# Kernel tuning notes

Measured on AMD Instinct MI355X. Metric: run time of the kernel, lower is better.

Reference implementation:

```python
import jax, jax.numpy as jnp
import numpy as np

B, LP, LQ, H = 32, 2048, 512, 1024

def setup_inputs() -> dict:
    key = jax.random.key(0)
    k1, k2, k3, k4 = jax.random.split(key, 4)
    p_encode = jax.random.normal(k1, (B, LP, H), dtype=jnp.float32)
    q_encode = jax.random.normal(k2, (B, LQ, H), dtype=jnp.float32)
    # nn.Linear(H, H): weight [out, in], bias [out]
    bound = 1.0 / np.sqrt(H)
    G_weight = jax.random.uniform(k3, (H, H), dtype=jnp.float32, minval=-bound, maxval=bound)
    G_bias = jax.random.uniform(k4, (H,), dtype=jnp.float32, minval=-bound, maxval=bound)
    return {"p_encode": p_encode, "q_encode": q_encode, "G_weight": G_weight, "G_bias": G_bias}

def reference(p_encode, q_encode, G_weight, G_bias):
    # q_project = transpose(G(q_encode), -2, -1): [B, H, LQ]
    q_proj = jnp.einsum('bqh,oh->bqo', q_encode, G_weight) + G_bias  # [B, LQ, H]
    # att_matrix = bmm(p_encode, q_project^T): [B, LP, LQ]
    att = jnp.einsum('bph,bqh->bpq', p_encode, q_proj)
    # m_p = softmax over LQ (dim=-1) @ q_encode -> [B, LP, H]
    m_p = jnp.einsum('bpq,bqh->bph', jax.nn.softmax(att, axis=-1), q_encode)
    # m_q = softmax over LP (dim=-2), transposed, @ p_encode -> [B, LQ, H]
    m_q = jnp.einsum('bpq,bph->bqh', jax.nn.softmax(att, axis=-2), p_encode)
    return (m_p, m_q)
```

## Files before the change

### kernel.cpp

```cpp
#include <hip/hip_runtime.h>

typedef _Float16 half_t;
typedef _Float16 f16x8 __attribute__((ext_vector_type(8)));
typedef _Float16 f16x4 __attribute__((ext_vector_type(4)));
typedef float    f32x4 __attribute__((ext_vector_type(4)));
typedef float    f32x16 __attribute__((ext_vector_type(16)));

typedef const __attribute__((address_space(1))) void cg_void;
typedef __attribute__((address_space(3))) void lds_void;

#define BB 32
#define LP 2048
#define LQ 512
#define HH 1024

enum { M_QPROJ = 0, M_OUT32 = 1 };

__global__ void cvt16_k(const float* __restrict__ w, half_t* __restrict__ o) {
  long i = ((long)blockIdx.x * 256 + threadIdx.x) * 4;
  f32x4 v = *(const f32x4*)(w + i);
  f16x4 h;
  h[0] = (half_t)v[0]; h[1] = (half_t)v[1]; h[2] = (half_t)v[2]; h[3] = (half_t)v[3];
  *(f16x4*)(o + i) = h;
}

__global__ __launch_bounds__(256) void cvt2_k(const float* __restrict__ qe,
                                              half_t* __restrict__ q16o,
                                              half_t* __restrict__ qT16o,
                                              const float* __restrict__ pe,
                                              half_t* __restrict__ p16o,
                                              half_t* __restrict__ pT16o) {
  __shared__ half_t tile[64 * 64];
  const int byg = blockIdx.y;
  const float* in; half_t* rm; half_t* tr; int R, r0;
  if (byg < 8) { in = qe; rm = q16o; tr = qT16o; R = LQ; r0 = byg * 64; }
  else         { in = pe; rm = p16o; tr = pT16o; R = LP; r0 = (byg - 8) * 64; }
  const int C = HH;
  const long zb = blockIdx.z;
  const float* src = in + zb * (long)R * C;
  half_t* dstT = tr + zb * (long)C * R;
  half_t* dstR = rm + zb * (long)R * C;
  const int c0 = blockIdx.x * 64;
  const int t = threadIdx.x;
  const int cl = (t & 15) * 4;
  const int rl = t >> 4;
#pragma unroll
  for (int rr = 0; rr < 4; rr++) {
    int r = rr * 16 + rl;
    f32x4 v = *(const f32x4*)(src + (long)(r0 + r) * C + c0 + cl);
    f16x4 h;
#pragma unroll
    for (int j = 0; j < 4; j++) {
      h[j] = (half_t)v[j];
      int c = cl + j;
      tile[c * 64 + (r ^ (((c >> 3) & 7) << 3))] = h[j];
    }
    *(f16x4*)(dstR + (long)(r0 + r) * C + c0 + cl) = h;
  }
  __syncthreads();
  const int c = t >> 2;
  const int rch = (t & 3) * 16;
  const int m = (c >> 3) & 7;
  const int B0 = c * 64 + (rch ^ ((m << 3) & 48));
  const int hi = (m & 1) << 3;
  f16x8 g0 = *(const f16x8*)&tile[B0 + hi];
  f16x8 g1 = *(const f16x8*)&tile[B0 + (8 ^ hi)];
  half_t* dp = dstT + (long)(c0 + c) * R + r0 + rch;
  *(f16x8*)dp = g0;
  *(f16x8*)(dp + 8) = g1;
}

__global__ __launch_bounds__(256) void cfin_k(const float* __restrict__ pmg,
                                              const float* __restrict__ psg,
                                              float* __restrict__ cmax,
                                              float* __restrict__ cinv) {
  long i = (long)blockIdx.x * 256 + threadIdx.x;
  long b = i / LQ, q = i - b * LQ;
  const float* mp = pmg + (b * 16) * LQ + q;
  const float* sp = psg + (b * 16) * LQ + q;
  float m = -3e38f, s = 0.f;
#pragma unroll
  for (int t = 0; t < 16; t++) {
    float mm = mp[(long)t * LQ], ss = sp[(long)t * LQ];
    float nm = fmaxf(m, mm);
    s = s * __expf(m - nm) + ss * __expf(mm - nm);
    m = nm;
  }
  cmax[i] = m;
  cinv[i] = 1.f / s;
}

__global__ __launch_bounds__(256) void pq_k(const half_t* __restrict__ E,
                                            half_t* __restrict__ out,
                                            const float* __restrict__ pmg,
                                            const float* __restrict__ cmax,
                                            const float* __restrict__ cinv) {
  __shared__ half_t tile[64 * 64];
  const long zb = blockIdx.z;
  const half_t* src = E + zb * (long)LP * LQ;
  half_t* dst = out + zb * (long)LQ * LP;
  const int r0 = blockIdx.y * 64, c0 = blockIdx.x * 64;
  const int tIdx = r0 >> 7;
  const int t = threadIdx.x;
  const int cl = (t & 15) * 4;
  const int rl = t >> 4;
  f32x4 tm = *(const f32x4*)(pmg + ((long)zb * 16 + tIdx) * LQ + c0 + cl);
  f32x4 cm = *(const f32x4*)(cmax + (long)zb * LQ + c0 + cl);
  f32x4 ci = *(const f32x4*)(cinv + (long)zb * LQ + c0 + cl);
  float sc[4];
#pragma unroll
  for (int j = 0; j < 4; j++) sc[j] = __expf(tm[j] - cm[j]) * ci[j];
#pragma unroll
  for (int rr = 0; rr < 4; rr++) {
    int r = rr * 16 + rl;
    f16x4 v = *(const f16x4*)(src + (long)(r0 + r) * LQ + c0 + cl);
#pragma unroll
    for (int j = 0; j < 4; j++) {
      float x = (float)v[j] * sc[j];
      int c = cl + j;
      tile[c * 64 + (r ^ (((c >> 3) & 7) << 3))] = (half_t)x;
    }
  }
  __syncthreads();
  const int c = t >> 2;
  const int rch = (t & 3) * 16;
  const int m = (c >> 3) & 7;
  const int B0 = c * 64 + (rch ^ ((m << 3) & 48));
  const int hi = (m & 1) << 3;
  f16x8 g0 = *(const f16x8*)&tile[B0 + hi];
  f16x8 g1 = *(const f16x8*)&tile[B0 + (8 ^ hi)];
  half_t* dp = dst + (long)(c0 + c) * LP + r0 + rch;
  *(f16x8*)dp = g0;
  *(f16x8*)(dp + 8) = g1;
}

template<int ROWS>
__device__ __forceinline__ void stage_op(const half_t* src, int ld,
                                         half_t* lds_base, int wid, int lane) {
  const int goff = (((lane & 3) ^ ((lane >> 3) & 3)) << 3);
#pragma unroll
  for (int j = 0; j < ROWS / 128; ++j) {
    int row = j * 128 + wid * 16 + (lane >> 2);
    const half_t* g = src + (long)row * ld + goff;
    __builtin_amdgcn_global_load_lds((cg_void*)g,
        (lds_void*)(lds_base + j * 4096 + wid * 512), 16, 0, 0);
  }
}

__device__ __forceinline__ void xcd_swz(long lid, long nwg, long& out) {
  const long q8 = nwg >> 3, r8 = nwg & 7;
  const long xcd = lid & 7, rest = lid >> 3;
  out = (xcd < r8 ? xcd * (q8 + 1) : r8 * (q8 + 1) + (xcd - r8) * q8) + rest;
}

__global__ __launch_bounds__(512, 2) void attf_k(
    const half_t* __restrict__ Ap, const half_t* __restrict__ Bp,
    half_t* __restrict__ PpO, half_t* __restrict__ EO,
    float* __restrict__ pmg, float* __restrict__ psg) {
  __shared__ __align__(16) half_t As[3 * 4096];
  __shared__ __align__(16) half_t Bs[3 * 16384];
  __shared__ float rmL[4][128];
  __shared__ float cmL[2][512];
  __shared__ float rsL[4][128];
  __shared__ float csL[2][512];

  const int nby = gridDim.y;
  long lid;
  xcd_swz(blockIdx.y + (long)nby * blockIdx.z, (long)nby * gridDim.z, lid);
  const int by = (int)(lid % nby);
  const int bz = (int)(lid / nby);

  const int t0 = threadIdx.x;
  const int lane = t0 & 63;
  const int wid = t0 >> 6;
  const int wm = wid >> 2, wn = wid & 3;
  const int m0 = by * 128;

  const half_t* Abase = Ap + ((long)bz * LP + m0) * HH;
  const half_t* Bbase = Bp + (long)bz * LQ * HH;

  const int c5 = lane & 31, hi = lane >> 5;
  const int sx = (c5 >> 1) & 3;
  const int ofs0 = c5 * 32 + ((hi ^ sx) << 3);
  const int ofs1 = c5 * 32 + (((2 | hi) ^ sx) << 3);

  f32x16 acc[2][4] = {};
  const int NT = HH / 32;

#pragma unroll
  for (int tt = 0; tt < 2; ++tt) {
    stage_op<128>(Abase + tt * 32, HH, As + tt * 4096, wid, lane);
    stage_op<512>(Bbase + tt * 32, HH, Bs + tt * 16384, wid, lane);
  }

  for (int t = 0; t < NT; ++t) {
    if (t + 1 < NT) asm volatile("s_waitcnt vmcnt(5)" ::: "memory");
    else            asm volatile("s_waitcnt vmcnt(0)" ::: "memory");
    __builtin_amdgcn_s_barrier();
    asm volatile("" ::: "memory");

    const half_t* Au = As + (t % 3) * 4096;
    const half_t* Bu = Bs + (t % 3) * 16384;
    f16x8 af[2][2], bf[4][2];
#pragma unroll
    for (int mf = 0; mf < 2; ++mf) {
      const half_t* p = Au + (wm * 64 + mf * 32) * 32;
      af[mf][0] = *(const f16x8*)(p + ofs0);
      af[mf][1] = *(const f16x8*)(p + ofs1);
    }
#pragma unroll
    for (int nf = 0; nf < 4; ++nf) {
      const half_t* p = Bu + (wn * 128 + nf * 32) * 32;
      bf[nf][0] = *(const f16x8*)(p + ofs0);
      bf[nf][1] = *(const f16x8*)(p + ofs1);
    }
    if (t + 2 < NT) {
      const int u2 = (t + 2) % 3;
      stage_op<128>(Abase + (t + 2) * 32, HH, As + u2 * 4096, wid, lane);
      stage_op<512>(Bbase + (t + 2) * 32, HH, Bs + u2 * 16384, wid, lane);
    }
    __builtin_amdgcn_s_setprio(1);
#pragma unroll
    for (int mf = 0; mf < 2; ++mf)
#pragma unroll
      for (int nf = 0; nf < 4; ++nf) {
        acc[mf][nf] = __builtin_amdgcn_mfma_f32_32x32x16_f16(af[mf][0], bf[nf][0], acc[mf][nf], 0, 0, 0);
        acc[mf][nf] = __builtin_amdgcn_mfma_f32_32x32x16_f16(af[mf][1], bf[nf][1], acc[mf][nf], 0, 0, 0);
      }
    __builtin_amdgcn_s_setprio(0);
  }

  float rmv[2][16], cmv[4];
#pragma unroll
  for (int m = 0; m < 2; ++m)
#pragma unroll
    for (int r = 0; r < 16; ++r) {
      float v = fmaxf(fmaxf(acc[m][0][r], acc[m][1][r]), fmaxf(acc[m][2][r], acc[m][3][r]));
#pragma unroll
      for (int o = 1; o < 32; o <<= 1) v = fmaxf(v, __shfl_xor(v, o, 64));
      rmv[m][r] = v;
    }
#pragma unroll
  for (int n = 0; n < 4; ++n) {
    float v = acc[0][n][0];
#pragma unroll
    for (int m = 0; m < 2; ++m)
#pragma unroll
      for (int r = 0; r < 16; ++r) v = fmaxf(v, acc[m][n][r]);
    v = fmaxf(v, __shfl_xor(v, 32, 64));
    cmv[n] = v;
  }
  if (c5 < 16) {
#pragma unroll
    for (int m = 0; m < 2; ++m)
      rmL[wn][wm * 64 + m * 32 + (c5 & 3) + 8 * (c5 >> 2) + 4 * hi] = rmv[m][c5];
  }
  if (hi == 0) {
#pragma unroll
    for (int n = 0; n < 4; ++n) cmL[wm][wn * 128 + n * 32 + c5] = cmv[n];
  }
  __syncthreads();
  if (t0 < 128)
    rmL[0][t0] = fmaxf(fmaxf(rmL[0][t0], rmL[1][t0]), fmaxf(rmL[2][t0], rmL[3][t0]));
  {
    float cm2 = fmaxf(cmL[0][t0 & 511], cmL[1][t0 & 511]);
    cmL[0][t0 & 511] = cm2;
    pmg[((long)bz * 16 + by) * LQ + (t0 & 511)] = cm2;
  }
  __syncthreads();
#pragma unroll
  for (int m = 0; m < 2; ++m)
#pragma unroll
    for (int r = 0; r < 16; ++r)
      rmv[m][r] = rmL[0][wm * 64 + m * 32 + (r & 3) + 8 * (r >> 2) + 4 * hi];
#pragma unroll
  for (int n = 0; n < 4; ++n) cmv[n] = cmL[0][wn * 128 + n * 32 + c5];

  half_t* EB = EO + (long)bz * LP * LQ;
  float csW[4] = {0.f, 0.f, 0.f, 0.f};
  float rowS[2][16];
#pragma unroll
  for (int m = 0; m < 2; ++m)
#pragma unroll
    for (int r = 0; r < 16; ++r) {
      long grow = (long)(m0 + wm * 64 + m * 32 + (r & 3) + 8 * (r >> 2) + 4 * hi) * LQ;
      float s = 0.f;
#pragma unroll
      for (int n = 0; n < 4; ++n) {
        float a = acc[m][n][r];
        float e = __expf(a - cmv[n]);
        float p = __expf(a - rmv[m][r]);
        csW[n] += e;
        EB[grow + wn * 128 + n * 32 + c5] = (half_t)e;
        acc[m][n][r] = p;
        s += p;
      }
#pragma unroll
      for (int o = 1; o < 32; o <<= 1) s += __shfl_xor(s, o, 64);
      rowS[m][r] = s;
    }
#pragma unroll
  for (int n = 0; n < 4; ++n) csW[n] += __shfl_xor(csW[n], 32, 64);
  if (c5 < 16) {
#pragma unroll
    for (int m = 0; m < 2; ++m)
      rsL[wn][wm * 64 + m * 32 + (c5 & 3) + 8 * (c5 >> 2) + 4 * hi] = rowS[m][c5];
  }
  if (hi == 0) {
#pragma unroll
    for (int n = 0; n < 4; ++n) csL[wm][wn * 128 + n * 32 + c5] = csW[n];
  }
  __syncthreads();
  if (t0 < 128)
    rsL[0][t0] = 1.f / (rsL[0][t0] + rsL[1][t0] + rsL[2][t0] + rsL[3][t0]);
  psg[((long)bz * 16 + by) * LQ + (t0 & 511)] = csL[0][t0 & 511] + csL[1][t0 & 511];
  __syncthreads();

  half_t* PpB = PpO + (long)bz * LP * LQ;
#pragma unroll
  for (int m = 0; m < 2; ++m)
#pragma unroll
    for (int r = 0; r < 16; ++r) {
      int row = wm * 64 + m * 32 + (r & 3) + 8 * (r >> 2) + 4 * hi;
      long grow = (long)(m0 + row) * LQ;
      float ri = rsL[0][row];
#pragma unroll
      for (int n = 0; n < 4; ++n)
        PpB[grow + wn * 128 + n * 32 + c5] = (half_t)(acc[m][n][r] * ri);
    }
}

template<int MODE>
__device__ __forceinline__ void core8(const half_t* __restrict__ Ab,
                                      const half_t* __restrict__ Bb,
                                      void* __restrict__ cB,
                                      const float* __restrict__ biasB,
                                      int lda, int ldb, int ldc, int K) {
  __shared__ __align__(16) half_t As[3][8192];
  __shared__ __align__(16) half_t Bs[3][8192];

  const int t0 = threadIdx.x;
  const int lane = t0 & 63;
  const int wid = t0 >> 6;
  const int wm = wid >> 2, wn = wid & 3;
  const int fr = lane & 15, fs = lane >> 4;
  const int fbase = fr * 32 + ((fs ^ ((fr >> 1) & 3)) << 3);

  f32x4 acc[8][4] = {};
  const int NT = K >> 5;

  stage_op<256>(Ab, lda, As[0], wid, lane);
  stage_op<256>(Bb, ldb, Bs[0], wid, lane);
  stage_op<256>(Ab + 32, lda, As[1], wid, lane);
  stage_op<256>(Bb + 32, ldb, Bs[1], wid, lane);
  asm volatile("s_waitcnt vmcnt(4)" ::: "memory");
  __builtin_amdgcn_s_barrier();
  asm volatile("" ::: "memory");

  for (int t = 0; t < NT; ++t) {
    const half_t* Au = As[t % 3];
    const half_t* Bu = Bs[t % 3];
    f16x8 af[4], bf[4], ag[4];
#pragma unroll
    for (int mf = 0; mf < 4; ++mf)
      af[mf] = *(const f16x8*)&Au[(wm * 128 + mf * 16) * 32 + fbase];
#pragma unroll
    for (int nf = 0; nf < 4; ++nf)
      bf[nf] = *(const f16x8*)&Bu[(wn * 64 + nf * 16) * 32 + fbase];
    if (t + 2 < NT) stage_op<256>(Ab + (t + 2) * 32, lda, As[(t + 2) % 3], wid, lane);
    __builtin_amdgcn_s_barrier();
    asm volatile("" ::: "memory");
    __builtin_amdgcn_s_setprio(1);
#pragma unroll
    for (int mf = 0; mf < 4; ++mf)
#pragma unroll
      for (int nf = 0; nf < 4; ++nf)
        acc[mf][nf] = __builtin_amdgcn_mfma_f32_16x16x32_f16(af[mf], bf[nf], acc[mf][nf], 0, 0, 0);
    __builtin_amdgcn_s_setprio(0);
    __builtin_amdgcn_s_barrier();
    asm volatile("" ::: "memory");
#pragma unroll
    for (int mf = 0; mf < 4; ++mf)
      ag[mf] = *(const f16x8*)&Au[(wm * 128 + 64 + mf * 16) * 32 + fbase];
    if (t + 2 < NT) stage_op<256>(Bb + (t + 2) * 32, ldb, Bs[(t + 2) % 3], wid, lane);
    __builtin_amdgcn_s_setprio(1);
#pragma unroll
    for (int mf = 0; mf < 4; ++mf)
#pragma unroll
      for (int nf = 0; nf < 4; ++nf)
        acc[4 + mf][nf] = __builtin_amdgcn_mfma_f32_16x16x32_f16(ag[mf], bf[nf], acc[4 + mf][nf], 0, 0, 0);
    __builtin_amdgcn_s_setprio(0);
    if (t + 2 < NT)      asm volatile("s_waitcnt vmcnt(4)" ::: "memory");
    else if (t + 1 < NT) asm volatile("s_waitcnt vmcnt(0)" ::: "memory");
    __builtin_amdgcn_s_barrier();
    asm volatile("" ::: "memory");
  }

  const int r0 = (lane >> 4) * 4;
#pragma unroll
  for (int nf = 0; nf < 4; ++nf) {
    int col = wn * 64 + nf * 16 + fr;
    float bv = 0.f;
    if constexpr (MODE == M_QPROJ) bv = biasB[col];
#pragma unroll
    for (int i = 0; i < 8; ++i) {
      int row = wm * 128 + (i >> 2) * 64 + (i & 3) * 16 + r0;
#pragma unroll
      for (int j = 0; j < 4; j++) {
        if constexpr (MODE == M_QPROJ)
          ((half_t*)cB)[(long)(row + j) * ldc + col] = (half_t)(acc[i][nf][j] + bv);
        else
          ((float*)cB)[(long)(row + j) * ldc + col] = acc[i][nf][j];
      }
    }
  }
}

__global__ __launch_bounds__(512, 2) void gemmq_k(const half_t* __restrict__ q16,
                                                  const half_t* __restrict__ w16,
                                                  half_t* __restrict__ qpj,
                                                  const float* __restrict__ Gb) {
  long lid;
  xcd_swz(blockIdx.x + 4L * blockIdx.y, 4L * gridDim.y, lid);
  const int bx = (int)(lid % 4);
  const int by = (int)(lid / 4);
  core8<M_QPROJ>(q16 + (long)(by * 256) * HH,
                 w16 + (long)(bx * 256) * HH,
                 qpj + (long)(by * 256) * HH + bx * 256,
                 Gb + bx * 256, HH, HH, HH, HH);
}

__global__ __launch_bounds__(512, 2) void gemm2_k(
    const half_t* __restrict__ Pp, const half_t* __restrict__ qT16, float* __restrict__ m_p,
    const half_t* __restrict__ Pq, const half_t* __restrict__ pT16, float* __restrict__ m_q) {
  long lid;
  xcd_swz(blockIdx.x + 4L * (blockIdx.y + 10L * blockIdx.z), 4L * 10 * 32, lid);
  const int bx = (int)(lid % 4);
  const long tmp = lid / 4;
  const int by = (int)(tmp % 10);
  const int bz = (int)(tmp / 10);

  if (by < 2) {
    core8<M_OUT32>(Pq + (long)bz * LQ * LP + (long)(by * 256) * LP,
                   pT16 + (long)bz * HH * LP + (long)(bx * 256) * LP,
                   m_q + (long)bz * LQ * HH + (long)(by * 256) * HH + bx * 256,
                   nullptr, LP, LP, HH, LP);
  } else {
    const int py = by - 2;
    core8<M_OUT32>(Pp + (long)bz * LP * LQ + (long)(py * 256) * LQ,
                   qT16 + (long)bz * HH * LQ + (long)(bx * 256) * LQ,
                   m_p + (long)bz * LP * HH + (long)(py * 256) * HH + bx * 256,
                   nullptr, LQ, LQ, HH, LQ);
  }
}

extern "C" void kernel_launch(void* const* d_in, const int* in_sizes, int n_in,
                              void* d_out, int out_size, void* d_ws, size_t ws_size,
                              hipStream_t stream) {
  const float* p_enc = (const float*)d_in[0];
  const float* q_enc = (const float*)d_in[1];
  const float* Gw    = (const float*)d_in[2];
  const float* Gb    = (const float*)d_in[3];
  float* m_p = (float*)d_out;
  float* m_q = m_p + (long)BB * LP * HH;

  half_t* w16   = (half_t*)d_ws;
  half_t* q16   = w16 + (long)HH * HH;
  half_t* qT16  = q16 + (long)BB * LQ * HH;
  half_t* qpj16 = qT16 + (long)BB * HH * LQ;
  half_t* p16   = qpj16 + (long)BB * LQ * HH;
  half_t* pT16  = p16 + (long)BB * LP * HH;
  half_t* Pp    = pT16 + (long)BB * HH * LP;
  half_t* Ebuf  = Pp + (long)BB * LP * LQ;
  half_t* Pq    = Ebuf + (long)BB * LP * LQ;
  float*  cmaxb = (float*)(Pq + (long)BB * LQ * LP);
  float*  cinvb = cmaxb + (long)BB * LQ;
  float*  pmg   = cinvb + (long)BB * LQ;
  float*  psg   = pmg + (long)BB * 16 * LQ;

  cvt16_k<<<HH * HH / 1024, 256, 0, stream>>>(Gw, w16);

  cvt2_k<<<dim3(HH / 64, 40, BB), 256, 0, stream>>>(q_enc, q16, qT16, p_enc, p16, pT16);

  gemmq_k<<<dim3(4, 64, 1), 512, 0, stream>>>(q16, w16, qpj16, Gb);

  attf_k<<<dim3(1, LP / 128, BB), 512, 0, stream>>>(p16, qpj16, Pp, Ebuf, pmg, psg);

  cfin_k<<<BB * LQ / 256, 256, 0, stream>>>(pmg, psg, cmaxb, cinvb);
  pq_k<<<dim3(LQ / 64, LP / 64, BB), 256, 0, stream>>>(Ebuf, Pq, pmg, cmaxb, cinvb);

  gemm2_k<<<dim3(4, 10, BB), 512, 0, stream>>>(Pp, qT16, m_p, Pq, pT16, m_q);
}
```

Baseline: 564.9 us.

## Rework GEMM mainloop into 8-slot quarter-tile pipeline with K=64 stages

Replaces the 3-stage K=32 double-operand pipeline with an 8-slot LDS ring of half-tiles staged at K=64. Loads are issued in quarter-steps interleaved with four MFMA phases per iteration. LDS grows to 128KB per block, so launch bounds drop to one block per CU. The aim is deeper prefetch and finer-grained overlap of global-to-LDS loads with MFMA, at the cost of occupancy and more barriers per iteration.

```diff
diff --git a/kernel.cpp b/kernel.cpp
--- a/kernel.cpp
+++ b/kernel.cpp
@@ -330,109 +330,145 @@
     }
 }
 
+__device__ __forceinline__ void stage_half(const half_t* src, int ld, int k0,
+                                           half_t* slot, int half_id, int wid, int lane) {
+#pragma unroll
+  for (int j = 0; j < 2; ++j) {
+    int c = j * 512 + wid * 64 + lane;
+    int lr = c >> 3, sl = c & 7;
+    int gr = (lr & 63) + half_id * 64 + (lr >> 6) * 128;
+    const half_t* g = src + (long)gr * ld + k0 + (((sl ^ (lr & 7))) << 3);
+    __builtin_amdgcn_global_load_lds((cg_void*)g,
+        (lds_void*)(slot + j * 4096 + wid * 512), 16, 0, 0);
+  }
+}
+
+__device__ __forceinline__ void stage_s(int s, const half_t* Ab, const half_t* Bb,
+                                        int lda, int ldb, half_t* lds, int NT,
+                                        int wid, int lane) {
+  int ts = s >> 2;
+  if (ts >= NT) return;
+  int kind = s & 3;
+  half_t* slot = lds + (s & 7) * 8192;
+  int k0 = ts * 64;
+  if (kind == 0)      stage_half(Ab, lda, k0, slot, 0, wid, lane);
+  else if (kind == 1) stage_half(Bb, ldb, k0, slot, 0, wid, lane);
+  else if (kind == 2) stage_half(Bb, ldb, k0, slot, 1, wid, lane);
+  else                stage_half(Ab, lda, k0, slot, 1, wid, lane);
+}
+
 template<int MODE>
-__device__ __forceinline__ void core8(const half_t* __restrict__ Ab,
-                                      const half_t* __restrict__ Bb,
-                                      void* __restrict__ cB,
-                                      const float* __restrict__ biasB,
-                                      int lda, int ldb, int ldc, int K) {
-  __shared__ __align__(16) half_t As[3][8192];
-  __shared__ __align__(16) half_t Bs[3][8192];
-
+__device__ __forceinline__ void core8p(const half_t* __restrict__ Ab,
+                                       const half_t* __restrict__ Bb,
+                                       void* __restrict__ cB,
+                                       const float* __restrict__ biasB,
+                                       int lda, int ldb, int ldc, int K,
+                                       half_t* lds) {
   const int t0 = threadIdx.x;
   const int lane = t0 & 63;
   const int wid = t0 >> 6;
   const int wm = wid >> 2, wn = wid & 3;
   const int fr = lane & 15, fs = lane >> 4;
-  const int fbase = fr * 32 + ((fs ^ ((fr >> 1) & 3)) << 3);
 
   f32x4 acc[8][4] = {};
-  const int NT = K >> 5;
-
-  stage_op<256>(Ab, lda, As[0], wid, lane);
-  stage_op<256>(Bb, ldb, Bs[0], wid, lane);
-  stage_op<256>(Ab + 32, lda, As[1], wid, lane);
-  stage_op<256>(Bb + 32, ldb, Bs[1], wid, lane);
+  const int NT = K >> 6;
+
+#pragma unroll
+  for (int s = 0; s < 5; ++s) stage_s(s, Ab, Bb, lda, ldb, lds, NT, wid, lane);
   asm volatile("s_waitcnt vmcnt(4)" ::: "memory");
   __builtin_amdgcn_s_barrier();
   asm volatile("" ::: "memory");
 
   for (int t = 0; t < NT; ++t) {
-    const half_t* Au = As[t % 3];
-    const half_t* Bu = Bs[t % 3];
-    f16x8 af[4], bf[4], ag[4];
-#pragma unroll
-    for (int mf = 0; mf < 4; ++mf)
-      af[mf] = *(const f16x8*)&Au[(wm * 128 + mf * 16) * 32 + fbase];
-#pragma unroll
-    for (int nf = 0; nf < 4; ++nf)
-      bf[nf] = *(const f16x8*)&Bu[(wn * 64 + nf * 16) * 32 + fbase];
-    if (t + 2 < NT) stage_op<256>(Ab + (t + 2) * 32, lda, As[(t + 2) % 3], wid, lane);
-    __builtin_amdgcn_s_barrier();
-    asm volatile("" ::: "memory");
-    __builtin_amdgcn_s_setprio(1);
-#pragma unroll
-    for (int mf = 0; mf < 4; ++mf)
-#pragma unroll
-      for (int nf = 0; nf < 4; ++nf)
-        acc[mf][nf] = __builtin_amdgcn_mfma_f32_16x16x32_f16(af[mf], bf[nf], acc[mf][nf], 0, 0, 0);
-    __builtin_amdgcn_s_setprio(0);
-    __builtin_amdgcn_s_barrier();
-    asm volatile("" ::: "memory");
-#pragma unroll
-    for (int mf = 0; mf < 4; ++mf)
-      ag[mf] = *(const f16x8*)&Au[(wm * 128 + 64 + mf * 16) * 32 + fbase];
-    if (t + 2 < NT) stage_op<256>(Bb + (t + 2) * 32, ldb, Bs[(t + 2) % 3], wid, lane);
-    __builtin_amdgcn_s_setprio(1);
-#pragma unroll
-    for (int mf = 0; mf < 4; ++mf)
-#pragma unroll
-      for (int nf = 0; nf < 4; ++nf)
-        acc[4 + mf][nf] = __builtin_amdgcn_mfma_f32_16x16x32_f16(ag[mf], bf[nf], acc[4 + mf][nf], 0, 0, 0);
-    __builtin_amdgcn_s_setprio(0);
-    if (t + 2 < NT)      asm volatile("s_waitcnt vmcnt(4)" ::: "memory");
-    else if (t + 1 < NT) asm volatile("s_waitcnt vmcnt(0)" ::: "memory");
-    __builtin_amdgcn_s_barrier();
-    asm volatile("" ::: "memory");
-  }
-
-  const int r0 = (lane >> 4) * 4;
+    const int base4 = 4 * t;
+    const half_t* slotA0 = lds + ((base4) & 7) * 8192;
+    const half_t* slotB0 = lds + ((base4 + 1) & 7) * 8192;
+    const half_t* slotB1 = lds + ((base4 + 2) & 7) * 8192;
+    const half_t* slotA1 = lds + ((base4 + 3) & 7) * 8192;
+    const bool drain = (t + 2 >= NT);
+    f16x8 bf[4][2];
+#pragma unroll
+    for (int p = 0; p < 4; ++p) {
+      f16x8 af[2][2];
+      const half_t* aslot = (p < 2) ? slotA0 : slotA1;
+      const int lrbase = wm * 64 + (p & 1) * 32;
+#pragma unroll
+      for (int i = 0; i < 2; ++i) {
+        int lr = lrbase + i * 16 + fr;
+#pragma unroll
+        for (int kh = 0; kh < 2; ++kh)
+          af[i][kh] = *(const f16x8*)&aslot[lr * 64 + (((fs + 4 * kh) ^ (lr & 7)) << 3)];
+      }
+      if (p == 0) {
+        const half_t* bslot = (wn & 1) ? slotB1 : slotB0;
+#pragma unroll
+        for (int nf = 0; nf < 4; ++nf) {
+          int lr = (wn >> 1) * 64 + nf * 16 + fr;
+#pragma unroll
+          for (int kh = 0; kh < 2; ++kh)
+            bf[nf][kh] = *(const f16x8*)&bslot[lr * 64 + (((fs + 4 * kh) ^ (lr & 7)) << 3)];
+        }
+      }
+      stage_s(base4 + p + 5, Ab, Bb, lda, ldb, lds, NT, wid, lane);
+      if (drain) asm volatile("s_waitcnt vmcnt(0)" ::: "memory");
+      else       asm volatile("s_waitcnt vmcnt(4)" ::: "memory");
+      __builtin_amdgcn_s_barrier();
+      asm volatile("s_waitcnt lgkmcnt(0)" ::: "memory");
+      __builtin_amdgcn_sched_barrier(0);
+      __builtin_amdgcn_s_setprio(1);
+#pragma unroll
+      for (int kh = 0; kh < 2; ++kh)
+#pragma unroll
+        for (int i = 0; i < 2; ++i)
+#pragma unroll
+          for (int nf = 0; nf < 4; ++nf)
+            acc[p * 2 + i][nf] =
+                __builtin_amdgcn_mfma_f32_16x16x32_f16(af[i][kh], bf[nf][kh], acc[p * 2 + i][nf], 0, 0, 0);
+      __builtin_amdgcn_s_setprio(0);
+      __builtin_amdgcn_s_barrier();
+      asm volatile("" ::: "memory");
+    }
+  }
+
+  const int r0 = fs * 4;
 #pragma unroll
   for (int nf = 0; nf < 4; ++nf) {
     int col = wn * 64 + nf * 16 + fr;
     float bv = 0.f;
     if constexpr (MODE == M_QPROJ) bv = biasB[col];
 #pragma unroll
-    for (int i = 0; i < 8; ++i) {
-      int row = wm * 128 + (i >> 2) * 64 + (i & 3) * 16 + r0;
+    for (int mf = 0; mf < 8; ++mf) {
+      int row = wm * 128 + (mf >> 2) * 64 + ((mf >> 1) & 1) * 32 + (mf & 1) * 16 + r0;
 #pragma unroll
       for (int j = 0; j < 4; j++) {
         if constexpr (MODE == M_QPROJ)
-          ((half_t*)cB)[(long)(row + j) * ldc + col] = (half_t)(acc[i][nf][j] + bv);
+          ((half_t*)cB)[(long)(row + j) * ldc + col] = (half_t)(acc[mf][nf][j] + bv);
         else
-          ((float*)cB)[(long)(row + j) * ldc + col] = acc[i][nf][j];
+          ((float*)cB)[(long)(row + j) * ldc + col] = acc[mf][nf][j];
       }
     }
   }
 }
 
-__global__ __launch_bounds__(512, 2) void gemmq_k(const half_t* __restrict__ q16,
+__global__ __launch_bounds__(512, 1) void gemmq_k(const half_t* __restrict__ q16,
                                                   const half_t* __restrict__ w16,
                                                   half_t* __restrict__ qpj,
                                                   const float* __restrict__ Gb) {
+  __shared__ __align__(16) half_t lds[8 * 8192];
   long lid;
   xcd_swz(blockIdx.x + 4L * blockIdx.y, 4L * gridDim.y, lid);
   const int bx = (int)(lid % 4);
   const int by = (int)(lid / 4);
-  core8<M_QPROJ>(q16 + (long)(by * 256) * HH,
-                 w16 + (long)(bx * 256) * HH,
-                 qpj + (long)(by * 256) * HH + bx * 256,
-                 Gb + bx * 256, HH, HH, HH, HH);
-}
-
-__global__ __launch_bounds__(512, 2) void gemm2_k(
+  core8p<M_QPROJ>(q16 + (long)(by * 256) * HH,
+                  w16 + (long)(bx * 256) * HH,
+                  qpj + (long)(by * 256) * HH + bx * 256,
+                  Gb + bx * 256, HH, HH, HH, HH, lds);
+}
+
+__global__ __launch_bounds__(512, 1) void gemm2_k(
     const half_t* __restrict__ Pp, const half_t* __restrict__ qT16, float* __restrict__ m_p,
     const half_t* __restrict__ Pq, const half_t* __restrict__ pT16, float* __restrict__ m_q) {
+  __shared__ __align__(16) half_t lds[8 * 8192];
   long lid;
   xcd_swz(blockIdx.x + 4L * (blockIdx.y + 10L * blockIdx.z), 4L * 10 * 32, lid);
   const int bx = (int)(lid % 4);
@@ -441,16 +477,16 @@
   const int bz = (int)(tmp / 10);
 
   if (by < 2) {
-    core8<M_OUT32>(Pq + (long)bz * LQ * LP + (long)(by * 256) * LP,
-                   pT16 + (long)bz * HH * LP + (long)(bx * 256) * LP,
-                   m_q + (long)bz * LQ * HH + (long)(by * 256) * HH + bx * 256,
-                   nullptr, LP, LP, HH, LP);
+    core8p<M_OUT32>(Pq + (long)bz * LQ * LP + (long)(by * 256) * LP,
+                    pT16 + (long)bz * HH * LP + (long)(bx * 256) * LP,
+                    m_q + (long)bz * LQ * HH + (long)(by * 256) * HH + bx * 256,
+                    nullptr, LP, LP, HH, LP, lds);
   } else {
     const int py = by - 2;
-    core8<M_OUT32>(Pp + (long)bz * LP * LQ + (long)(py * 256) * LQ,
-                   qT16 + (long)bz * HH * LQ + (long)(bx * 256) * LQ,
-                   m_p + (long)bz * LP * HH + (long)(py * 256) * HH + bx * 256,
-                   nullptr, LQ, LQ, HH, LQ);
+    core8p<M_OUT32>(Pp + (long)bz * LP * LQ + (long)(py * 256) * LQ,
+                    qT16 + (long)bz * HH * LQ + (long)(bx * 256) * LQ,
+                    m_p + (long)bz * LP * HH + (long)(py * 256) * HH + bx * 256,
+                    nullptr, LQ, LQ, HH, LQ, lds);
   }
 }
 
```

New measurement: 515.6 us. -8.7%, faster.
